# Optimization experiments

Hardware: AMD Instinct MI355X
Metric: run time of the kernel (lower is better)

Reference implementation:

```python
import jax, jax.numpy as jnp
import numpy as np

L = 4          # GAT_LAYERS
HEADS = 4      # N_HEADS
H = 64         # transformer hidden dim
DH = H // HEADS
FIN = 32       # NODE_EMBED_SIZE
A = 15         # gats.num_actions (readout size)
OBS = 1500     # flattened obs dim
HS = 512       # hidden_size (policy FC)
NOUT = 15      # num_outputs
VH = 128       # VALUE_HIDDENS
B = 128        # batch of graphs
N = 1000       # nodes per map graph
TOT = B * N
DEG = 4
E = TOT * DEG


def _lin(key, fan_in, shape):
    return jax.random.normal(key, shape, jnp.float32) * (1.0 / np.sqrt(fan_in))


def setup_inputs() -> dict:
    key = jax.random.key(0)
    ks = jax.random.split(key, 30)
    node_feats = jax.random.normal(ks[0], (TOT, FIN), jnp.float32)
    obs = jax.random.normal(ks[1], (B, OBS), jnp.float32)
    # batched-graph edges: endpoints stay within each graph (DGL batch semantics)
    off = (jnp.arange(B) * N)[:, None]
    edge_src = (jax.random.randint(ks[2], (B, N * DEG), 0, N) + off).reshape(-1).astype(jnp.int32)
    edge_dst = (jax.random.randint(ks[3], (B, N * DEG), 0, N) + off).reshape(-1).astype(jnp.int32)
    agent_nodes = (jax.random.randint(ks[4], (B,), 0, N) + jnp.arange(B) * N).astype(jnp.int32)
    p = {
        'W_in': _lin(ks[5], FIN, (FIN, H)),
        'Wq': _lin(ks[6], H, (L, H, H)), 'Wk': _lin(ks[7], H, (L, H, H)),
        'Wv': _lin(ks[8], H, (L, H, H)), 'Wo': _lin(ks[9], H, (L, H, H)),
        'ln1_g': jnp.ones((L, H), jnp.float32), 'ln1_b': jnp.zeros((L, H), jnp.float32),
        'W1': _lin(ks[10], H, (L, H, 2 * H)), 'b1': jnp.zeros((L, 2 * H), jnp.float32),
        'W2': _lin(ks[11], 2 * H, (L, 2 * H, H)), 'b2': jnp.zeros((L, H), jnp.float32),
        'ln2_g': jnp.ones((L, H), jnp.float32), 'ln2_b': jnp.zeros((L, H), jnp.float32),
        'Wr': _lin(ks[12], H, (H, A)), 'br': jnp.zeros((A,), jnp.float32),
        'Wp1': _lin(ks[13], A + OBS, (A + OBS, HS)), 'bp1': jnp.zeros((HS,), jnp.float32),
        'Wp2': _lin(ks[14], HS, (HS, HS)), 'bp2': jnp.zeros((HS,), jnp.float32),
        'Wlog': _lin(ks[15], HS, (HS, NOUT)), 'blog': jnp.zeros((NOUT,), jnp.float32),
        'Wv1': _lin(ks[16], OBS, (OBS, VH)), 'bv1': jnp.zeros((VH,), jnp.float32),
        'Wv2': _lin(ks[17], VH, (VH, VH)), 'bv2': jnp.zeros((VH,), jnp.float32),
        'Wvo': _lin(ks[18], VH, (VH, 1)), 'bvo': jnp.zeros((1,), jnp.float32),
    }
    return dict(node_feats=node_feats, obs=obs, edge_src=edge_src, edge_dst=edge_dst,
                agent_nodes=agent_nodes, **p)


def _layernorm(x, g, b):
    m = x.mean(-1, keepdims=True)
    v = ((x - m) ** 2).mean(-1, keepdims=True)
    return (x - m) * jax.lax.rsqrt(v + 1e-5) * g + b


def reference(node_feats, obs, edge_src, edge_dst, agent_nodes, W_in, Wq, Wk, Wv, Wo,
              ln1_g, ln1_b, W1, b1, W2, b2, ln2_g, ln2_b, Wr, br,
              Wp1, bp1, Wp2, bp2, Wlog, blog, Wv1, bv1, Wv2, bv2, Wvo, bvo):
    n = node_feats.shape[0]
    x = node_feats @ W_in                                   # [n, H]
    inv_sqrt_dh = np.float32(1.0 / np.sqrt(DH))
    for l in range(L):
        q = (x @ Wq[l]).reshape(n, HEADS, DH)
        k = (x @ Wk[l]).reshape(n, HEADS, DH)
        v = (x @ Wv[l]).reshape(n, HEADS, DH)
        # per-edge attention scores, softmax over incoming edges of each dst node
        s = jnp.sum(q[edge_dst] * k[edge_src], axis=-1) * inv_sqrt_dh   # [E, HEADS]
        m = jax.ops.segment_max(s, edge_dst, num_segments=n)            # [n, HEADS]
        w = jnp.exp(s - m[edge_dst])
        denom = jax.ops.segment_sum(w, edge_dst, num_segments=n)        # [n, HEADS]
        agg = jax.ops.segment_sum(w[:, :, None] * v[edge_src], edge_dst, num_segments=n)
        attn = (agg / (denom[:, :, None] + 1e-9)).reshape(n, H) @ Wo[l]
        x = _layernorm(x + attn, ln1_g[l], ln1_b[l])
        h = jax.nn.relu(x @ W1[l] + b1[l]) @ W2[l] + b2[l]
        x = _layernorm(x + h, ln2_g[l], ln2_b[l])
    gat_out = x[agent_nodes] @ Wr + br                      # [B, A] per-agent action features
    feat = jnp.tanh(jnp.concatenate([gat_out, obs], axis=1) @ Wp1 + bp1)
    feat = jnp.tanh(feat @ Wp2 + bp2)
    logits = feat @ Wlog + blog                             # [B, NOUT]
    vh = jnp.tanh(obs @ Wv1 + bv1)
    vh = jnp.tanh(vh @ Wv2 + bv2)
    value = (vh @ Wvo + bvo)[:, 0]                          # [B]
    return logits, value
```

## Files before the change

### kernel.cpp

```cpp
#include <hip/hip_runtime.h>
#include <hip/hip_bf16.h>
#include <cstdint>
#include <cstddef>

#define DEV static __device__ __forceinline__

constexpr int GRAPHS = 128;
constexpr int NPG    = 1000;
constexpr int EPG    = 4000;
constexpr int TOTN   = GRAPHS * NPG;
constexpr int TOTE   = GRAPHS * EPG;
constexpr int HD     = 64;
constexpr int OBSD   = 1500;
constexpr int AD     = 15;

typedef __attribute__((ext_vector_type(8))) short bf16x8;
typedef __attribute__((ext_vector_type(4))) float f32x4;

DEV unsigned short f2b(float f){
  unsigned u = __float_as_uint(f);
  return (unsigned short)((u + 0x7fffu + ((u >> 16) & 1u)) >> 16);
}
DEV float b2f(unsigned short s){ return __uint_as_float((unsigned)s << 16); }

DEV void fma4(float4& a, float s, const float4 w){
  a.x = fmaf(s, w.x, a.x); a.y = fmaf(s, w.y, a.y);
  a.z = fmaf(s, w.z, a.z); a.w = fmaf(s, w.w, a.w);
}

DEV ushort4 pack4(float4 v){
  ushort4 r; r.x=f2b(v.x); r.y=f2b(v.y); r.z=f2b(v.z); r.w=f2b(v.w); return r;
}

__global__ __launch_bounds__(256) void k_wprep(const float* __restrict__ Wq,
    const float* __restrict__ Wk, const float* __restrict__ Wv,
    const float* __restrict__ Wo, const float* __restrict__ W1,
    const float* __restrict__ W2, unsigned short* __restrict__ wpack){
  int e = blockIdx.x*256 + threadIdx.x;
  int l = e >> 15;
  int r = e & 32767;
  float val;
  if (r < 12288){
    int c = r >> 6, k = r & 63;
    val = (c < 64)  ? Wq[l*4096 + k*64 + c]
        : (c < 128) ? Wk[l*4096 + k*64 + (c-64)]
                    : Wv[l*4096 + k*64 + (c-128)];
  } else if (r < 16384){
    int i = r - 12288; int c = i >> 6, k = i & 63;
    val = Wo[l*4096 + k*64 + c];
  } else if (r < 24576){
    int i = r - 16384; int c = i >> 6, k = i & 63;
    val = W1[l*8192 + k*128 + c];
  } else {
    int i = r - 24576; int c = i >> 7, k = i & 127;
    val = W2[l*8192 + k*64 + c];
  }
  wpack[e] = f2b(val);
}

__global__ __launch_bounds__(256) void k_zero(int* __restrict__ cnt){
  cnt[blockIdx.x*256 + threadIdx.x] = 0;
}

__global__ __launch_bounds__(256) void k_hist(const int* __restrict__ edst,
                                              int* __restrict__ cnt){
  int e = blockIdx.x*256 + threadIdx.x;
  atomicAdd(&cnt[edst[e]], 1);
}

__global__ __launch_bounds__(1024) void k_scan(const int* __restrict__ cnt,
    int* __restrict__ rstart, int* __restrict__ cursor){
  __shared__ int s[1024];
  const int g = blockIdx.x, tid = threadIdx.x;
  int v = (tid < NPG) ? cnt[g*NPG + tid] : 0;
  s[tid] = v;
  __syncthreads();
  #pragma unroll
  for (int off=1; off<1024; off<<=1){
    int t = (tid >= off) ? s[tid-off] : 0;
    __syncthreads();
    s[tid] += t;
    __syncthreads();
  }
  if (tid < NPG){
    int r = g*EPG + (s[tid] - v);
    rstart[g*NPG+tid] = r;
    cursor[g*NPG+tid] = r;
  }
}

__global__ __launch_bounds__(256) void k_scatter(const int* __restrict__ esrc,
    const int* __restrict__ edst, int* __restrict__ cursor,
    int* __restrict__ esorted){
  int e = blockIdx.x*256 + threadIdx.x;
  int pos = atomicAdd(&cursor[edst[e]], 1);
  esorted[pos] = esrc[e];
}

__global__ __launch_bounds__(256) void k_in(const float* __restrict__ nf,
                                            const float* __restrict__ Win,
                                            unsigned short* __restrict__ xb){
  __shared__ float  s_nf[256*36];
  __shared__ float4 s_w[512];
  const int tid = threadIdx.x;
  const int node0 = blockIdx.x * 256;
  const float4* W4 = (const float4*)Win;
  s_w[tid] = W4[tid]; s_w[tid+256] = W4[tid+256];
  const float4* nf4 = (const float4*)nf;
  float4* snf4 = (float4*)s_nf;
  #pragma unroll
  for (int r=0;r<8;r++){
    int i = tid + 256*r; int n = i>>3, k4 = i&7;
    snf4[n*9 + k4] = nf4[(size_t)(node0+n)*8 + k4];
  }
  __syncthreads();
  const int ng = tid>>2, cg = tid&3;
  float4 acc[4][4];
  #pragma unroll
  for (int i=0;i<4;i++){ acc[i][0]=make_float4(0,0,0,0); acc[i][1]=make_float4(0,0,0,0);
                         acc[i][2]=make_float4(0,0,0,0); acc[i][3]=make_float4(0,0,0,0); }
  #pragma unroll 4
  for (int k=0;k<32;k++){
    float nv[4];
    #pragma unroll
    for (int i=0;i<4;i++) nv[i] = s_nf[(ng + 64*i)*36 + k];
    float4 w[4];
    #pragma unroll
    for (int j=0;j<4;j++) w[j] = s_w[k*16 + cg*4 + j];
    #pragma unroll
    for (int i=0;i<4;i++){
      #pragma unroll
      for (int j=0;j<4;j++) fma4(acc[i][j], nv[i], w[j]);
    }
  }
  ushort4* xb4 = (ushort4*)xb;
  #pragma unroll
  for (int i=0;i<4;i++){
    size_t nidx = (size_t)(node0 + ng + 64*i) * 16;
    #pragma unroll
    for (int j=0;j<4;j++) xb4[nidx + cg*4 + j] = pack4(acc[i][j]);
  }
}

__global__ __launch_bounds__(256) void k_qkv_m(const unsigned short* __restrict__ xb,
    const unsigned short* __restrict__ wqkvT,
    unsigned short* __restrict__ qkv){
  __shared__ short s_w[192*72];
  __shared__ short s_st[4][16*104];
  const int tid = threadIdx.x;
  const int node0 = blockIdx.x * 256;
  {
    const unsigned* src = (const unsigned*)wqkvT;
    unsigned* dst = (unsigned*)s_w;
    #pragma unroll
    for (int r=0;r<24;r++){
      int j = tid + 256*r;
      int c = j >> 5, kk = j & 31;
      dst[c*36 + kk] = src[j];
    }
  }
  __syncthreads();
  const int lane = tid & 63, wave = tid >> 6;
  const int m = lane & 15, quad = lane >> 4;
  const int rowbase = node0 + wave*64;
  bf16x8 af[4][2];
  #pragma unroll
  for (int rt=0;rt<4;rt++){
    const unsigned short* xp = xb + (size_t)(rowbase + rt*16 + m)*64 + quad*8;
    af[rt][0] = *(const bf16x8*)xp;
    af[rt][1] = *(const bf16x8*)(xp + 32);
  }
  short* st = s_st[wave];
  #pragma unroll
  for (int rt=0;rt<4;rt++){
    #pragma unroll
    for (int half=0; half<2; half++){
      #pragma unroll
      for (int c6=0;c6<6;c6++){
        int ct = half*6 + c6;
        bf16x8 b0 = *(const bf16x8*)&s_w[(ct*16+m)*72 + quad*8];
        bf16x8 b1 = *(const bf16x8*)&s_w[(ct*16+m)*72 + 32 + quad*8];
        f32x4 acc = {0.f,0.f,0.f,0.f};
        acc = __builtin_amdgcn_mfma_f32_16x16x32_bf16(af[rt][0], b0, acc, 0,0,0);
        acc = __builtin_amdgcn_mfma_f32_16x16x32_bf16(af[rt][1], b1, acc, 0,0,0);
        #pragma unroll
        for (int i=0;i<4;i++)
          st[(quad*4+i)*104 + c6*16 + m] = (short)f2b(acc[i]);
      }
      #pragma unroll
      for (int j=0;j<3;j++){
        int flat = (j*64 + lane)*8;
        int r = flat / 96, c = flat % 96;
        bf16x8 v = *(const bf16x8*)&st[r*104 + c];
        *(bf16x8*)(qkv + (size_t)(rowbase + rt*16 + r)*192 + half*96 + c) = v;
      }
    }
  }
}

__global__ __launch_bounds__(256) void k_edge2(const unsigned short* __restrict__ qkv,
    const int* __restrict__ rstart, const int* __restrict__ cnt,
    const int* __restrict__ esorted, unsigned short* __restrict__ attn_in){
  const int tid = threadIdx.x;
  const int wb = (blockIdx.x & 7)*1000 + (blockIdx.x >> 3);
  const int lane = tid & 63;
  const int sub  = lane >> 4;
  const int dg   = lane & 15;
  const int wave = tid >> 6;
  const int node = wb*16 + wave*4 + sub;
  ushort4 qu = *(const ushort4*)(qkv + (size_t)node*192 + dg*4);
  float q0 = b2f(qu.x), q1 = b2f(qu.y), q2 = b2f(qu.z), q3 = b2f(qu.w);
  const int rs = rstart[node];
  const int n  = cnt[node];
  const int nn = min(n, 16);
  int myidx = (dg < nn) ? esorted[rs + dg] : node;
  const int lbase = lane & 48;
  float a0=0.f, a1=0.f, a2=0.f, a3=0.f, den=0.f;
  ushort4 kA, vA, kB, vB;
  if (nn > 0){
    int s0 = __shfl(myidx, lbase);
    kA = *(const ushort4*)(qkv + (size_t)s0*192 + 64 + dg*4);
    vA = *(const ushort4*)(qkv + (size_t)s0*192 + 128 + dg*4);
  }
  if (nn > 1){
    int s1 = __shfl(myidx, lbase + 1);
    kB = *(const ushort4*)(qkv + (size_t)s1*192 + 64 + dg*4);
    vB = *(const ushort4*)(qkv + (size_t)s1*192 + 128 + dg*4);
  }
  for (int i=0;i<nn;i++){
    ushort4 ck = kA, cv = vA;
    kA = kB; vA = vB;
    if (i+2 < nn){
      int s2 = __shfl(myidx, lbase + i + 2);
      kB = *(const ushort4*)(qkv + (size_t)s2*192 + 64 + dg*4);
      vB = *(const ushort4*)(qkv + (size_t)s2*192 + 128 + dg*4);
    }
    float p = q0*b2f(ck.x) + q1*b2f(ck.y) + q2*b2f(ck.z) + q3*b2f(ck.w);
    p += __shfl_xor(p, 1);
    p += __shfl_xor(p, 2);
    float w = __expf(p * 0.25f);
    den += w;
    a0 = fmaf(w, b2f(cv.x), a0);
    a1 = fmaf(w, b2f(cv.y), a1);
    a2 = fmaf(w, b2f(cv.z), a2);
    a3 = fmaf(w, b2f(cv.w), a3);
  }
  for (int i=16;i<n;i++){
    int src = esorted[rs + i];
    ushort4 ku = *(const ushort4*)(qkv + (size_t)src*192 + 64 + dg*4);
    ushort4 vu = *(const ushort4*)(qkv + (size_t)src*192 + 128 + dg*4);
    float p = q0*b2f(ku.x) + q1*b2f(ku.y) + q2*b2f(ku.z) + q3*b2f(ku.w);
    p += __shfl_xor(p, 1);
    p += __shfl_xor(p, 2);
    float w = __expf(p * 0.25f);
    den += w;
    a0 = fmaf(w, b2f(vu.x), a0);
    a1 = fmaf(w, b2f(vu.y), a1);
    a2 = fmaf(w, b2f(vu.z), a2);
    a3 = fmaf(w, b2f(vu.w), a3);
  }
  float inv = 1.0f/(den + 1e-9f);
  ushort4 o;
  o.x = f2b(a0*inv); o.y = f2b(a1*inv); o.z = f2b(a2*inv); o.w = f2b(a3*inv);
  ((ushort4*)attn_in)[(size_t)node*16 + dg] = o;
}

__global__ __launch_bounds__(256) void k_attn_ffn(
    const unsigned short* __restrict__ attn_in,
    unsigned short* __restrict__ xb,
    const unsigned short* __restrict__ woT,
    const unsigned short* __restrict__ w1T, const float* __restrict__ b1_l,
    const unsigned short* __restrict__ w2T, const float* __restrict__ b2_l,
    const float* __restrict__ l1g, const float* __restrict__ l1b,
    const float* __restrict__ l2g, const float* __restrict__ l2b){
  __shared__ short s_w1[128*72];
  __shared__ short s_w2[64*136];
  __shared__ short s_st[4][16*136];
  const int tid = threadIdx.x;
  const int node0 = blockIdx.x*256;
  {
    const unsigned* src = (const unsigned*)w1T;
    unsigned* dst = (unsigned*)s_w1;
    #pragma unroll
    for (int r=0;r<16;r++){
      int j = tid + 256*r;
      int c = j >> 5, kk = j & 31;
      dst[c*36 + kk] = src[j];
    }
  }
  {
    const unsigned* src = (const unsigned*)w2T;
    unsigned* dst = (unsigned*)s_w2;
    #pragma unroll
    for (int r=0;r<16;r++){
      int j = tid + 256*r;
      int c = j >> 6, kk = j & 63;
      dst[c*68 + kk] = src[j];
    }
  }
  const int lane = tid&63, wave = tid>>6;
  const int m = lane&15, quad = lane>>4;
  const int rowbase = node0 + wave*64;
  bf16x8 wo[4][2];
  #pragma unroll
  for (int ct=0;ct<4;ct++){
    wo[ct][0] = *(const bf16x8*)&woT[(ct*16+m)*64 + quad*8];
    wo[ct][1] = *(const bf16x8*)&woT[(ct*16+m)*64 + 32 + quad*8];
  }
  float g1[4], bb1[4], g2[4], bb2[4], b2v[4];
  #pragma unroll
  for (int ct=0;ct<4;ct++){
    g1[ct]=l1g[ct*16+m]; bb1[ct]=l1b[ct*16+m];
    g2[ct]=l2g[ct*16+m]; bb2[ct]=l2b[ct*16+m];
    b2v[ct]=b2_l[ct*16+m];
  }
  float b1v[8];
  #pragma unroll
  for (int ct=0;ct<8;ct++) b1v[ct]=b1_l[ct*16+m];
  bf16x8 af[4][2];
  #pragma unroll
  for (int rt=0;rt<4;rt++){
    const unsigned short* ap = attn_in + (size_t)(rowbase + rt*16 + m)*64 + quad*8;
    af[rt][0] = *(const bf16x8*)ap;
    af[rt][1] = *(const bf16x8*)(ap + 32);
  }
  __syncthreads();
  short* st = s_st[wave];
  #pragma unroll
  for (int rt=0;rt<4;rt++){
    f32x4 acc[4];
    #pragma unroll
    for (int ct=0;ct<4;ct++){
      f32x4 z = {0.f,0.f,0.f,0.f};
      z = __builtin_amdgcn_mfma_f32_16x16x32_bf16(af[rt][0], wo[ct][0], z, 0,0,0);
      z = __builtin_amdgcn_mfma_f32_16x16x32_bf16(af[rt][1], wo[ct][1], z, 0,0,0);
      acc[ct] = z;
    }
    float x1v[4][4];
    #pragma unroll
    for (int i=0;i<4;i++){
      size_t row = (size_t)(rowbase + rt*16 + quad*4 + i)*64;
      float v0 = acc[0][i] + b2f(xb[row + m]);
      float v1 = acc[1][i] + b2f(xb[row + 16 + m]);
      float v2 = acc[2][i] + b2f(xb[row + 32 + m]);
      float v3 = acc[3][i] + b2f(xb[row + 48 + m]);
      float sm = v0+v1+v2+v3;
      float sq = v0*v0+v1*v1+v2*v2+v3*v3;
      #pragma unroll
      for (int mk=1; mk<16; mk<<=1){ sm += __shfl_xor(sm, mk); sq += __shfl_xor(sq, mk); }
      float mean = sm*0.015625f;
      float var  = sq*0.015625f - mean*mean;
      float rs   = rsqrtf(var + 1e-5f);
      x1v[i][0] = (v0-mean)*rs*g1[0]+bb1[0];
      x1v[i][1] = (v1-mean)*rs*g1[1]+bb1[1];
      x1v[i][2] = (v2-mean)*rs*g1[2]+bb1[2];
      x1v[i][3] = (v3-mean)*rs*g1[3]+bb1[3];
      int rl = quad*4 + i;
      st[rl*136 + m]      = (short)f2b(x1v[i][0]);
      st[rl*136 + 16 + m] = (short)f2b(x1v[i][1]);
      st[rl*136 + 32 + m] = (short)f2b(x1v[i][2]);
      st[rl*136 + 48 + m] = (short)f2b(x1v[i][3]);
    }
    bf16x8 x10 = *(const bf16x8*)&st[m*136 + quad*8];
    bf16x8 x11 = *(const bf16x8*)&st[m*136 + 32 + quad*8];
    #pragma unroll
    for (int ct=0;ct<8;ct++){
      bf16x8 b0 = *(const bf16x8*)&s_w1[(ct*16+m)*72 + quad*8];
      bf16x8 b1 = *(const bf16x8*)&s_w1[(ct*16+m)*72 + 32 + quad*8];
      f32x4 z = {0.f,0.f,0.f,0.f};
      z = __builtin_amdgcn_mfma_f32_16x16x32_bf16(x10, b0, z, 0,0,0);
      z = __builtin_amdgcn_mfma_f32_16x16x32_bf16(x11, b1, z, 0,0,0);
      #pragma unroll
      for (int i=0;i<4;i++)
        st[(quad*4+i)*136 + ct*16 + m] = (short)f2b(fmaxf(z[i]+b1v[ct], 0.f));
    }
    bf16x8 h0 = *(const bf16x8*)&st[m*136 + quad*8];
    bf16x8 h1 = *(const bf16x8*)&st[m*136 + 32 + quad*8];
    bf16x8 h2 = *(const bf16x8*)&st[m*136 + 64 + quad*8];
    bf16x8 h3 = *(const bf16x8*)&st[m*136 + 96 + quad*8];
    f32x4 acc2[4];
    #pragma unroll
    for (int ct=0;ct<4;ct++){
      f32x4 z = {0.f,0.f,0.f,0.f};
      z = __builtin_amdgcn_mfma_f32_16x16x32_bf16(h0, *(const bf16x8*)&s_w2[(ct*16+m)*136 + quad*8],      z, 0,0,0);
      z = __builtin_amdgcn_mfma_f32_16x16x32_bf16(h1, *(const bf16x8*)&s_w2[(ct*16+m)*136 + 32 + quad*8], z, 0,0,0);
      z = __builtin_amdgcn_mfma_f32_16x16x32_bf16(h2, *(const bf16x8*)&s_w2[(ct*16+m)*136 + 64 + quad*8], z, 0,0,0);
      z = __builtin_amdgcn_mfma_f32_16x16x32_bf16(h3, *(const bf16x8*)&s_w2[(ct*16+m)*136 + 96 + quad*8], z, 0,0,0);
      acc2[ct] = z;
    }
    #pragma unroll
    for (int i=0;i<4;i++){
      float v0 = acc2[0][i] + b2v[0] + x1v[i][0];
      float v1 = acc2[1][i] + b2v[1] + x1v[i][1];
      float v2 = acc2[2][i] + b2v[2] + x1v[i][2];
      float v3 = acc2[3][i] + b2v[3] + x1v[i][3];
      float sm = v0+v1+v2+v3;
      float sq = v0*v0+v1*v1+v2*v2+v3*v3;
      #pragma unroll
      for (int mk=1; mk<16; mk<<=1){ sm += __shfl_xor(sm, mk); sq += __shfl_xor(sq, mk); }
      float mean = sm*0.015625f;
      float var  = sq*0.015625f - mean*mean;
      float rs   = rsqrtf(var + 1e-5f);
      int rl = quad*4 + i;
      st[rl*136 + m]      = (short)f2b((v0-mean)*rs*g2[0]+bb2[0]);
      st[rl*136 + 16 + m] = (short)f2b((v1-mean)*rs*g2[1]+bb2[1]);
      st[rl*136 + 32 + m] = (short)f2b((v2-mean)*rs*g2[2]+bb2[2]);
      st[rl*136 + 48 + m] = (short)f2b((v3-mean)*rs*g2[3]+bb2[3]);
    }
    #pragma unroll
    for (int j=0;j<2;j++){
      int flat = (j*64 + lane)*8;
      int r = flat >> 6, c = flat & 63;
      bf16x8 v = *(const bf16x8*)&st[r*136 + c];
      *(bf16x8*)(xb + (size_t)(rowbase + rt*16 + r)*64 + c) = v;
    }
  }
}

__global__ __launch_bounds__(512) void k_fc1(const unsigned short* __restrict__ xb,
    const float* __restrict__ obs, const int* __restrict__ agents,
    const float* __restrict__ Wr, const float* __restrict__ br,
    const float* __restrict__ Wp1, float* __restrict__ part1){
  constexpr int ROWS=2, COLS=256, CH=384, K=1515, N=512;
  const int chunk = 379;
  __shared__ float s_a[ROWS*CH];
  const int tid = threadIdx.x;
  const int ct = blockIdx.x, rg = blockIdx.y, ks = blockIdx.z;
  const int k0 = ks * chunk;
  const int len = min(K - k0, chunk);
  const int row0 = rg * ROWS;
  #pragma unroll
  for (int rr=0; rr<ROWS; rr++)
    for (int i=tid; i<len; i+=512){
      int k = k0 + i;
      if (k >= AD) s_a[rr*CH + i] = obs[(size_t)(row0+rr)*OBSD + (k-AD)];
    }
  if (ks==0 && tid < ROWS*AD){
    int rr = tid/AD, c = tid%AD;
    int b = row0 + rr;
    const unsigned short* xa = xb + (size_t)agents[b]*HD;
    float a = br[c];
    #pragma unroll 8
    for (int k=0;k<HD;k++) a = fmaf(b2f(xa[k]), Wr[k*AD + c], a);
    s_a[rr*CH + c] = a;
  }
  __syncthreads();
  const int r = tid / COLS, c = tid % COLS;
  const float* wp = Wp1 + (size_t)k0*N + ct*COLS + c;
  const float* ap = s_a + r*CH;
  float acc = 0.f;
  #pragma unroll 8
  for (int k=0;k<len;k++) acc = fmaf(ap[k], wp[(size_t)k*N], acc);
  part1[((size_t)ks*128 + row0 + r)*N + ct*COLS + c] = acc;
}

__global__ __launch_bounds__(512) void k_fc2(const float* __restrict__ part1,
    const float* __restrict__ bp1, const float* __restrict__ Wp2,
    float* __restrict__ part2){
  constexpr int ROWS=2, COLS=256, CH=256, N=512;
  __shared__ float s_a[ROWS*CH];
  const int tid = threadIdx.x;
  const int ct = blockIdx.x, rg = blockIdx.y, ks = blockIdx.z;
  const int k0 = ks * CH;
  const int row0 = rg * ROWS;
  #pragma unroll
  for (int rr=0; rr<ROWS; rr++)
    for (int i=tid; i<CH; i+=512){
      int k = k0 + i;
      float s = bp1[k];
      #pragma unroll
      for (int j=0;j<4;j++) s += part1[((size_t)j*128 + row0+rr)*512 + k];
      s_a[rr*CH + i] = tanhf(s);
    }
  __syncthreads();
  const int r = tid / COLS, c = tid % COLS;
  const float* wp = Wp2 + (size_t)k0*N + ct*COLS + c;
  const float* ap = s_a + r*CH;
  float acc = 0.f;
  #pragma unroll 8
  for (int k=0;k<CH;k++) acc = fmaf(ap[k], wp[(size_t)k*N], acc);
  part2[((size_t)ks*128 + row0 + r)*N + ct*COLS + c] = acc;
}

__global__ __launch_bounds__(256) void k_logits(const float* __restrict__ part2,
    const float* __restrict__ bp2, const float* __restrict__ Wlog,
    const float* __restrict__ blog, float* __restrict__ out){
  __shared__ float s_f[512];
  __shared__ float s_p[16*AD];
  const int b = blockIdx.x, tid = threadIdx.x;
  for (int i=tid;i<512;i+=256){
    float s = bp2[i] + part2[(size_t)b*512 + i] + part2[(size_t)(128+b)*512 + i];
    s_f[i] = tanhf(s);
  }
  __syncthreads();
  if (tid < 240){
    int c = tid % AD, kc = tid / AD;
    float a = 0.f;
    #pragma unroll 8
    for (int j=0;j<32;j++){ int k = kc*32 + j; a = fmaf(s_f[k], Wlog[k*AD + c], a); }
    s_p[tid] = a;
  }
  __syncthreads();
  if (tid < AD){
    float a = blog[tid];
    #pragma unroll
    for (int kc=0;kc<16;kc++) a += s_p[kc*AD + tid];
    out[(size_t)b*AD + tid] = a;
  }
}

template<int ROWS, int COLS, int CH, int KS, int N>
__global__ __launch_bounds__(ROWS*COLS) void k_gemm_part(
    const float* __restrict__ A, int lda, int K,
    const float* __restrict__ W, float* __restrict__ part){
  constexpr int BT = ROWS*COLS;
  __shared__ float s_a[ROWS*CH];
  const int tid = threadIdx.x;
  const int ct = blockIdx.x, rg = blockIdx.y, ks = blockIdx.z;
  const int chunk = (K + KS - 1) / KS;
  const int k0 = ks * chunk;
  const int len = min(K - k0, chunk);
  const int row0 = rg * ROWS;
  #pragma unroll
  for (int rr=0; rr<ROWS; rr++)
    for (int i=tid; i<len; i+=BT)
      s_a[rr*CH + i] = A[(size_t)(row0+rr)*lda + k0 + i];
  __syncthreads();
  const int r = tid / COLS, c = tid % COLS;
  const float* wp = W + (size_t)k0*N + ct*COLS + c;
  const float* ap = s_a + r*CH;
  float acc = 0.f;
  #pragma unroll 8
  for (int k=0;k<len;k++) acc = fmaf(ap[k], wp[(size_t)k*N], acc);
  part[((size_t)ks*128 + row0 + r)*N + ct*COLS + c] = acc;
}

__global__ __launch_bounds__(128) void k_vfin(const float* __restrict__ partv,
    const float* __restrict__ bv1, const float* __restrict__ Wv2,
    const float* __restrict__ bv2, const float* __restrict__ Wvo,
    const float* __restrict__ bvo, float* __restrict__ out){
  __shared__ float s_v[128];
  __shared__ float s_r[128];
  const int b = blockIdx.x, tid = threadIdx.x;
  {
    float s = bv1[tid];
    #pragma unroll
    for (int j=0;j<8;j++) s += partv[((size_t)j*128 + b)*128 + tid];
    s_v[tid] = tanhf(s);
  }
  __syncthreads();
  float a = bv2[tid];
  #pragma unroll 8
  for (int k=0;k<128;k++) a = fmaf(s_v[k], Wv2[k*128 + tid], a);
  s_r[tid] = tanhf(a) * Wvo[tid];
  __syncthreads();
  if (tid < 64){
    float v = s_r[tid] + s_r[tid+64];
    #pragma unroll
    for (int m=32;m>=1;m>>=1) v += __shfl_xor(v, m);
    if (tid==0) out[GRAPHS*AD + b] = v + bvo[0];
  }
}

extern "C" void kernel_launch(void* const* d_in, const int* in_sizes, int n_in,
                              void* d_out, int out_size, void* d_ws, size_t ws_size,
                              hipStream_t stream) {
  (void)in_sizes; (void)n_in; (void)out_size; (void)ws_size;
  const float* nf     = (const float*)d_in[0];
  const float* obs    = (const float*)d_in[1];
  const int*   esrc   = (const int*)d_in[2];
  const int*   edst   = (const int*)d_in[3];
  const int*   agents = (const int*)d_in[4];
  const float* Win    = (const float*)d_in[5];
  const float* Wq     = (const float*)d_in[6];
  const float* Wk     = (const float*)d_in[7];
  const float* Wv     = (const float*)d_in[8];
  const float* Wo     = (const float*)d_in[9];
  const float* ln1g   = (const float*)d_in[10];
  const float* ln1b   = (const float*)d_in[11];
  const float* W1     = (const float*)d_in[12];
  const float* b1     = (const float*)d_in[13];
  const float* W2     = (const float*)d_in[14];
  const float* b2     = (const float*)d_in[15];
  const float* ln2g   = (const float*)d_in[16];
  const float* ln2b   = (const float*)d_in[17];
  const float* Wr     = (const float*)d_in[18];
  const float* br     = (const float*)d_in[19];
  const float* Wp1    = (const float*)d_in[20];
  const float* bp1    = (const float*)d_in[21];
  const float* Wp2    = (const float*)d_in[22];
  const float* bp2    = (const float*)d_in[23];
  const float* Wlog   = (const float*)d_in[24];
  const float* blog   = (const float*)d_in[25];
  const float* Wv1    = (const float*)d_in[26];
  const float* bv1    = (const float*)d_in[27];
  const float* Wv2    = (const float*)d_in[28];
  const float* bv2    = (const float*)d_in[29];
  const float* Wvo    = (const float*)d_in[30];
  const float* bvo    = (const float*)d_in[31];
  float* out = (float*)d_out;

  unsigned short* xb      = (unsigned short*)d_ws;
  unsigned short* qkv     = xb + (size_t)TOTN*HD;
  unsigned short* attn_in = qkv + (size_t)TOTN*192;
  unsigned short* wpack   = attn_in + (size_t)TOTN*HD;
  int* cnt     = (int*)(wpack + 131072);
  int* rstart  = cnt + TOTN;
  int* cursor  = rstart + TOTN;
  int* esorted = cursor + TOTN;
  float* part1 = (float*)(esorted + TOTE);
  float* part2 = part1 + 4*128*512;
  float* partv = part2 + 2*128*512;

  k_wprep  <<<512, 256, 0, stream>>>(Wq, Wk, Wv, Wo, W1, W2, wpack);
  k_zero   <<<TOTN/256, 256, 0, stream>>>(cnt);
  k_hist   <<<TOTE/256, 256, 0, stream>>>(edst, cnt);
  k_scan   <<<GRAPHS, 1024, 0, stream>>>(cnt, rstart, cursor);
  k_scatter<<<TOTE/256, 256, 0, stream>>>(esrc, edst, cursor, esorted);

  k_in<<<TOTN/256, 256, 0, stream>>>(nf, Win, xb);
  for (int l=0; l<4; l++){
    const unsigned short* wl = wpack + l*32768;
    k_qkv_m   <<<TOTN/256, 256, 0, stream>>>(xb, wl, qkv);
    k_edge2   <<<TOTN/16, 256, 0, stream>>>(qkv, rstart, cnt, esorted, attn_in);
    k_attn_ffn<<<TOTN/256, 256, 0, stream>>>(attn_in, xb,
                                             wl + 12288,
                                             wl + 16384, b1 + l*128,
                                             wl + 24576, b2 + l*64,
                                             ln1g + l*64, ln1b + l*64,
                                             ln2g + l*64, ln2b + l*64);
  }
  k_fc1   <<<dim3(2,64,4), 512, 0, stream>>>(xb, obs, agents, Wr, br, Wp1, part1);
  k_fc2   <<<dim3(2,64,2), 512, 0, stream>>>(part1, bp1, Wp2, part2);
  k_logits<<<GRAPHS, 256, 0, stream>>>(part2, bp2, Wlog, blog, out);
  k_gemm_part<4,128,192,8,128><<<dim3(1,32,8), 512, 0, stream>>>(obs, 1500, 1500, Wv1, partv);
  k_vfin  <<<GRAPHS, 128, 0, stream>>>(partv, bv1, Wv2, bv2, Wvo, bvo, out);
}
```

Before: 486.4 us.

## Fuse next layer's QKV projection into attention/FFN kernel epilogue

The attention+FFN kernel now computes the next layer's Q/K/V projection from the freshly normalized tile still held in shared memory and writes qkv directly. This removes three separate QKV kernel launches and their re-read of the hidden state from global memory. The cost is extra MFMA work and weight loads from global memory (not staged in LDS) inside an already heavy kernel, which may raise register pressure. The first layer's QKV is still computed by the original kernel.

```diff
diff --git a/kernel.cpp b/kernel.cpp
--- a/kernel.cpp
+++ b/kernel.cpp
@@ -272,7 +272,9 @@
     const unsigned short* __restrict__ w1T, const float* __restrict__ b1_l,
     const unsigned short* __restrict__ w2T, const float* __restrict__ b2_l,
     const float* __restrict__ l1g, const float* __restrict__ l1b,
-    const float* __restrict__ l2g, const float* __restrict__ l2b){
+    const float* __restrict__ l2g, const float* __restrict__ l2b,
+    const unsigned short* __restrict__ wqkvT,
+    unsigned short* __restrict__ qkv){
   __shared__ short s_w1[128*72];
   __shared__ short s_w2[64*136];
   __shared__ short s_st[4][16*136];
@@ -413,6 +415,32 @@
       int r = flat >> 6, c = flat & 63;
       bf16x8 v = *(const bf16x8*)&st[r*136 + c];
       *(bf16x8*)(xb + (size_t)(rowbase + rt*16 + r)*64 + c) = v;
+    }
+    if (wqkvT){
+      bf16x8 x20 = *(const bf16x8*)&st[m*136 + quad*8];
+      bf16x8 x21 = *(const bf16x8*)&st[m*136 + 32 + quad*8];
+      #pragma unroll
+      for (int half=0; half<2; half++){
+        #pragma unroll
+        for (int c6=0;c6<6;c6++){
+          int ct = half*6 + c6;
+          bf16x8 b0 = *(const bf16x8*)&wqkvT[(ct*16+m)*64 + quad*8];
+          bf16x8 b1 = *(const bf16x8*)&wqkvT[(ct*16+m)*64 + 32 + quad*8];
+          f32x4 z = {0.f,0.f,0.f,0.f};
+          z = __builtin_amdgcn_mfma_f32_16x16x32_bf16(x20, b0, z, 0,0,0);
+          z = __builtin_amdgcn_mfma_f32_16x16x32_bf16(x21, b1, z, 0,0,0);
+          #pragma unroll
+          for (int i=0;i<4;i++)
+            st[(quad*4+i)*136 + c6*16 + m] = (short)f2b(z[i]);
+        }
+        #pragma unroll
+        for (int j=0;j<3;j++){
+          int flat = (j*64 + lane)*8;
+          int r = flat / 96, c = flat % 96;
+          bf16x8 v = *(const bf16x8*)&st[r*136 + c];
+          *(bf16x8*)(qkv + (size_t)(rowbase + rt*16 + r)*192 + half*96 + c) = v;
+        }
+      }
     }
   }
 }
@@ -619,16 +647,18 @@
   k_scatter<<<TOTE/256, 256, 0, stream>>>(esrc, edst, cursor, esorted);
 
   k_in<<<TOTN/256, 256, 0, stream>>>(nf, Win, xb);
+  k_qkv_m<<<TOTN/256, 256, 0, stream>>>(xb, wpack, qkv);
   for (int l=0; l<4; l++){
     const unsigned short* wl = wpack + l*32768;
-    k_qkv_m   <<<TOTN/256, 256, 0, stream>>>(xb, wl, qkv);
+    const unsigned short* wqkv_next = (l<3) ? (wpack + (l+1)*32768) : nullptr;
     k_edge2   <<<TOTN/16, 256, 0, stream>>>(qkv, rstart, cnt, esorted, attn_in);
     k_attn_ffn<<<TOTN/256, 256, 0, stream>>>(attn_in, xb,
                                              wl + 12288,
                                              wl + 16384, b1 + l*128,
                                              wl + 24576, b2 + l*64,
                                              ln1g + l*64, ln1b + l*64,
-                                             ln2g + l*64, ln2b + l*64);
+                                             ln2g + l*64, ln2b + l*64,
+                                             wqkv_next, qkv);
   }
   k_fc1   <<<dim3(2,64,4), 512, 0, stream>>>(xb, obs, agents, Wr, br, Wp1, part1);
   k_fc2   <<<dim3(2,64,2), 512, 0, stream>>>(part1, bp1, Wp2, part2);
```

Result: no change. 483.4 us (-0.6%).
